# Kernel tuning notes

Measured on AMD Instinct MI355X. Metric: run time of the kernel, lower is better.

Reference implementation:

```python
import jax, jax.numpy as jnp
import numpy as np

VOCAB = 100000
EMB = 300      # embd_dim
S = 40         # sequence_length
B = 8192
C = 210        # out_channels
KH = 3         # kernel_height
DH = 35        # dense_hidden
NC = 35        # n_classes
KPOOL = S - KH + 1          # 38: MaxPool2d kernel height
NBLK = C // KPOOL           # 5: pool blocks over the channel dim (last 20 chans dropped)


def setup_inputs() -> dict:
    key = jax.random.key(0)
    ks = jax.random.split(key, 9)
    return {
        "x": jax.random.randint(ks[0], (B, S), 0, VOCAB, dtype=jnp.int64 if jax.config.jax_enable_x64 else jnp.int32),
        "pos_": jax.random.randint(ks[1], (B, 2), 0, S, dtype=jnp.int64 if jax.config.jax_enable_x64 else jnp.int32),
        "w2v": jax.random.normal(ks[2], (VOCAB, EMB), jnp.float32) * 0.1,
        "conv_w": jax.random.normal(ks[3], (KH, EMB, C), jnp.float32) * 0.02,   # WIO layout
        "conv_b": jax.random.normal(ks[4], (C,), jnp.float32) * 0.02,
        "dense_w": jax.random.normal(ks[5], (3 * S, DH), jnp.float32) * 0.05,
        "dense_b": jax.random.normal(ks[6], (DH,), jnp.float32) * 0.05,
        "out_w": jax.random.normal(ks[7], (DH, NC), jnp.float32) * 0.05,
        "out_b": jax.random.normal(ks[8], (NC,), jnp.float32) * 0.05,
    }


def reference(x, pos_, w2v, conv_w, conv_b, dense_w, dense_b, out_w, out_b):
    # Embedding lookup: [B, S, EMB]
    emb = w2v[x]
    # Conv2d(1, C, (KH, EMB), padding=(1, 0)) == 1D conv over seq with full-width kernel
    c = jax.lax.conv_general_dilated(
        emb, conv_w, window_strides=(1,), padding=[(1, 1)],
        dimension_numbers=("NWC", "WIO", "NWC"))  # [B, S, C]
    c = jax.nn.relu(c + conv_b)
    c = jnp.transpose(c, (0, 2, 1))  # [B, C, S], matches conv.squeeze(3)

    # ep1/ep2 normalization (faithful to the python loop)
    ep1 = jnp.minimum(pos_[:, 0], pos_[:, 1])
    ep2 = jnp.maximum(pos_[:, 0], pos_[:, 1])
    shift = (ep1 == 0).astype(ep1.dtype)
    ep1 = ep1 + shift
    ep2 = ep2 + shift

    pos = jnp.arange(S)
    m1 = (pos[None, :] < ep1[:, None]).astype(c.dtype)                                  # before e1
    m2 = ((pos[None, :] >= ep1[:, None]) & (pos[None, :] < ep2[:, None])).astype(c.dtype)  # between
    m3 = (pos[None, :] >= ep2[:, None]).astype(c.dtype)                                 # after e2

    def pool(m):
        # mask along seq, then MaxPool2d((38,1)) on a 3D tensor pools the CHANNEL dim
        y = c * m[:, None, :]                                  # [B, C, S]
        y = y[:, : NBLK * KPOOL, :].reshape(y.shape[0], NBLK, KPOOL, S)
        return y.max(axis=2)                                   # [B, NBLK, S]

    pooled = jnp.concatenate([pool(m1), pool(m2), pool(m3)], axis=2)  # [B, NBLK, 3S]
    pooled = pooled.reshape(-1, 3 * S)                                # [NBLK*B, 3S]
    h = pooled @ dense_w + dense_b
    return h @ out_w + out_b  # [NBLK*B, NC]
```

## Files before the change

kernel.cpp:

```cpp
#include <hip/hip_runtime.h>

typedef short bf16x8 __attribute__((ext_vector_type(8)));
typedef float f32x4 __attribute__((ext_vector_type(4)));
typedef unsigned short u16;
typedef u16 ushort8v __attribute__((ext_vector_type(8)));

#define VOCAB 100000
#define EMB 300
#define SEQ 40
#define BATCH 8192
#define COUT 210
#define NBLK 5
#define KPOOL 38
#define DH 35
#define NCLS 35
#define PCOL 320
#define KDIM 960
#define NUSE 192
#define BM 80
#define EROWS 84
#define NGR 120

__device__ __forceinline__ u16 f2bf(float f) {
  unsigned u = __float_as_uint(f);
  unsigned r = 0x7FFFu + ((u >> 16) & 1u);
  return (u16)((u + r) >> 16);
}

__device__ __forceinline__ void gload_lds16(void* lds, const void* g) {
  __builtin_amdgcn_global_load_lds(
      (const __attribute__((address_space(1))) void*)g,
      (__attribute__((address_space(3))) void*)lds, 16, 0, 0);
}

__global__ __launch_bounds__(256) void k_prepW(const float* __restrict__ w2v,
                                               u16* __restrict__ W) {
  int id = blockIdx.x * 256 + threadIdx.x;
  if (id >= (VOCAB + 1) * 40) return;
  int v = id / 40, e8 = id - v * 40;
  int e = e8 * 8;
  float vals[8] = {0.f, 0.f, 0.f, 0.f, 0.f, 0.f, 0.f, 0.f};
  if (v < VOCAB) {
    const float* src = w2v + (size_t)v * EMB + e;
    if (e <= 292) {
      float4 f0 = *(const float4*)src;
      float4 f1 = *(const float4*)(src + 4);
      vals[0] = f0.x; vals[1] = f0.y; vals[2] = f0.z; vals[3] = f0.w;
      vals[4] = f1.x; vals[5] = f1.y; vals[6] = f1.z; vals[7] = f1.w;
    } else if (e == 296) {
      float4 f0 = *(const float4*)src;
      vals[0] = f0.x; vals[1] = f0.y; vals[2] = f0.z; vals[3] = f0.w;
    }
  }
  ushort8v o;
#pragma unroll
  for (int j = 0; j < 8; ++j) o[j] = f2bf(vals[j]);
  *(ushort8v*)(W + (size_t)v * PCOL + e) = o;
}

__global__ __launch_bounds__(256) void k_prepB(const float* __restrict__ convw,
                                               u16* __restrict__ Btn) {
  int id = blockIdx.x * 256 + threadIdx.x;
  if (id >= NGR * NUSE) return;
  int gg = id / NUSE, col = id - gg * NUSE;
  ushort8v o;
#pragma unroll
  for (int j = 0; j < 8; ++j) {
    int k = gg * 8 + j;
    int kh = (k >= 640) ? 2 : (k >= 320 ? 1 : 0);
    int e = k - kh * PCOL;
    float v = (e < EMB) ? convw[(kh * EMB + e) * COUT + col] : 0.f;
    o[j] = f2bf(v);
  }
  *(ushort8v*)(Btn + (size_t)id * 8) = o;
}

__global__ __launch_bounds__(256) void k_conv_gemm(const u16* __restrict__ Wb,
                                                   const u16* __restrict__ Btn,
                                                   const int* __restrict__ x,
                                                   const float* __restrict__ convb,
                                                   float* __restrict__ maxc) {
  __shared__ __align__(16) char smem[40 * EROWS * 16];
  float* act = (float*)smem;

  const int tid = threadIdx.x;
  const int lane = tid & 63;
  const int wc = tid >> 6;
  const int l15 = lane & 15, l4 = lane >> 4;
  const int m0 = blockIdx.x * BM;
  const int b0 = blockIdx.x * 2;

#pragma unroll
  for (int ri = 0; ri < 13; ++ri) {
    const int c = ri * 256 + tid;
    const int g = c / 84;
    const int prow = c - g * 84;
    const int bb = (prow >= 42) ? 1 : 0;
    const int sp = prow - 42 * bb;
    const int tok = (sp == 0 || sp == 41) ? VOCAB : x[(b0 + bb) * SEQ + sp - 1];
    gload_lds16(smem + c * 16, Wb + (size_t)tok * PCOL + g * 8);
  }
  if (tid < 32) {
    const int c = 3328 + tid;
    const int g = c / 84;
    const int prow = c - g * 84;
    const int bb = (prow >= 42) ? 1 : 0;
    const int sp = prow - 42 * bb;
    const int tok = (sp == 0 || sp == 41) ? VOCAB : x[(b0 + bb) * SEQ + sp - 1];
    gload_lds16(smem + c * 16, Wb + (size_t)tok * PCOL + g * 8);
  }
  __syncthreads();

  const int rA0 = l15;
  const int rA1 = 16 + l15;
  const int rA2 = 32 + l15 + ((l15 >= 8) ? 2 : 0);
  const int rA3 = 50 + l15;
  const int rA4 = 66 + l15;

  const u16* pbB = Btn + (size_t)((l4 * NUSE) + wc * 48 + l15) * 8;

  f32x4 acc[5][3];
  const f32x4 zero = {0.f, 0.f, 0.f, 0.f};
#pragma unroll
  for (int i = 0; i < 5; ++i)
#pragma unroll
    for (int j = 0; j < 3; ++j) acc[i][j] = zero;

  bf16x8 bs[3][3];

#define LOADB(SI, T)                                                           \
  {                                                                            \
    const u16* p_ = pbB + (size_t)(T) * 6144;                                  \
    bs[SI][0] = *(const bf16x8*)(p_);                                          \
    bs[SI][1] = *(const bf16x8*)(p_ + 128);                                    \
    bs[SI][2] = *(const bf16x8*)(p_ + 256);                                    \
  }

  LOADB(0, 0)
  LOADB(1, 1)

#pragma unroll
  for (int kh = 0; kh < 3; ++kh) {
#pragma unroll
    for (int kq = 0; kq < 10; ++kq) {
      const int t = kh * 10 + kq;
      if (t + 2 < 30) LOADB((t + 2) % 3, t + 2)
      const char* kb = smem + ((kq * 4 + l4) * EROWS + kh) * 16;
      bf16x8 a0 = *(const bf16x8*)(kb + rA0 * 16);
      bf16x8 a1 = *(const bf16x8*)(kb + rA1 * 16);
      bf16x8 a2 = *(const bf16x8*)(kb + rA2 * 16);
      bf16x8 a3 = *(const bf16x8*)(kb + rA3 * 16);
      bf16x8 a4 = *(const bf16x8*)(kb + rA4 * 16);
      __builtin_amdgcn_s_setprio(1);
#pragma unroll
      for (int fn = 0; fn < 3; ++fn) {
        acc[0][fn] = __builtin_amdgcn_mfma_f32_16x16x32_bf16(a0, bs[t % 3][fn], acc[0][fn], 0, 0, 0);
        acc[1][fn] = __builtin_amdgcn_mfma_f32_16x16x32_bf16(a1, bs[t % 3][fn], acc[1][fn], 0, 0, 0);
        acc[2][fn] = __builtin_amdgcn_mfma_f32_16x16x32_bf16(a2, bs[t % 3][fn], acc[2][fn], 0, 0, 0);
        acc[3][fn] = __builtin_amdgcn_mfma_f32_16x16x32_bf16(a3, bs[t % 3][fn], acc[3][fn], 0, 0, 0);
        acc[4][fn] = __builtin_amdgcn_mfma_f32_16x16x32_bf16(a4, bs[t % 3][fn], acc[4][fn], 0, 0, 0);
      }
      __builtin_amdgcn_s_setprio(0);
    }
  }
#undef LOADB

  __syncthreads();

#pragma unroll
  for (int fm = 0; fm < 5; ++fm) {
#pragma unroll
    for (int fn = 0; fn < 3; ++fn) {
      const int col = wc * 48 + fn * 16 + l15;
      const float bias = convb[col];
#pragma unroll
      for (int rg = 0; rg < 4; ++rg) {
        const int rloc = l4 * 4 + rg;
        float vv = acc[fm][fn][rg] + bias;
        act[rloc * 194 + col] = fmaxf(vv, 0.f);
      }
    }
    __syncthreads();
    if (tid < 80) {
      const int rl = tid / 5, gq = tid - rl * 5;
      const float* ap = act + rl * 194 + gq * KPOOL;
      float mx = 0.f;
#pragma unroll
      for (int i = 0; i < KPOOL; ++i) mx = fmaxf(mx, ap[i]);
      const int mloc = fm * 16 + rl;
      const int bb = (mloc >= 40) ? 1 : 0;
      const int ss = mloc - 40 * bb;
      maxc[((b0 + bb) * NBLK + gq) * SEQ + ss] = mx;
    }
    __syncthreads();
  }
}

__global__ __launch_bounds__(256) void k_dense(const float* __restrict__ maxc,
                                               const int* __restrict__ pos,
                                               const float* __restrict__ dw,
                                               const float* __restrict__ db,
                                               const float* __restrict__ ow,
                                               const float* __restrict__ ob,
                                               float* __restrict__ out) {
  __shared__ float dwL[120 * 36];
  __shared__ float owL[35 * 36];
  __shared__ float hL[64 * 36];
  __shared__ float mxL[64 * 40];
  const int tid = threadIdx.x;
  const int r0 = blockIdx.x * 64;
  for (int i = tid; i < 120 * 35; i += 256) { int j = i / 35, d = i - j * 35; dwL[j * 36 + d] = dw[i]; }
  for (int i = tid; i < 35 * 35; i += 256)  { int j = i / 35, d = i - j * 35; owL[j * 36 + d] = ow[i]; }
  for (int i = tid; i < 64 * 40; i += 256)  mxL[i] = maxc[(size_t)r0 * 40 + i];
  __syncthreads();
  for (int t = tid; t < 64 * 35; t += 256) {
    const int row = t / 35, d = t - row * 35;
    const int rg = r0 + row;
    const int b = rg / NBLK;
    const int p0 = pos[b * 2], p1 = pos[b * 2 + 1];
    int e1 = min(p0, p1), e2 = max(p0, p1);
    if (e1 == 0) { e1 = 1; e2 += 1; }
    float a = db[d];
#pragma unroll
    for (int s = 0; s < SEQ; ++s) {
      const int k = (s >= e1) + (s >= e2);
      a += mxL[row * 40 + s] * dwL[(k * SEQ + s) * 36 + d];
    }
    hL[row * 36 + d] = a;
  }
  __syncthreads();
  for (int t = tid; t < 64 * 35; t += 256) {
    const int row = t / 35, c = t - row * 35;
    float a = ob[c];
#pragma unroll
    for (int d = 0; d < DH; ++d) a += hL[row * 36 + d] * owL[d * 36 + c];
    out[(size_t)(r0 + row) * NCLS + c] = a;
  }
}

extern "C" void kernel_launch(void* const* d_in, const int* in_sizes, int n_in,
                              void* d_out, int out_size, void* d_ws, size_t ws_size,
                              hipStream_t stream) {
  const int*   x     = (const int*)d_in[0];
  const int*   pos   = (const int*)d_in[1];
  const float* w2v   = (const float*)d_in[2];
  const float* convw = (const float*)d_in[3];
  const float* convb = (const float*)d_in[4];
  const float* dw    = (const float*)d_in[5];
  const float* db    = (const float*)d_in[6];
  const float* ow    = (const float*)d_in[7];
  const float* ob    = (const float*)d_in[8];
  float* out = (float*)d_out;

  char* ws = (char*)d_ws;
  u16* W    = (u16*)ws;
  u16* Btn  = (u16*)(ws + 64000640);
  float* maxc = (float*)(ws + 64000640 + 368640);

  k_prepW<<<15626, 256, 0, stream>>>(w2v, W);
  k_prepB<<<90, 256, 0, stream>>>(convw, Btn);
  k_conv_gemm<<<4096, 256, 0, stream>>>(W, Btn, x, convb, maxc);
  k_dense<<<640, 256, 0, stream>>>(maxc, pos, dw, db, ow, ob, out);
}
```

Baseline: 182.3 us.

## Retile conv GEMM to 128-row blocks with 32x32x16 MFMA and 8 waves

Restructures the conv GEMM kernel so each 512-thread block covers 128 output rows (spanning up to 5 batch items) instead of 80 rows. Each of the 8 waves now computes a 32x96 tile with 32x32x16 bf16 MFMAs, holding 3 accumulators instead of 15. A fragments are double-buffered from LDS and B fragments are prefetched from global memory two steps ahead. The aim is more reuse per A/B load and fewer, larger MFMA instructions. In exchange the LDS staging footprint roughly doubles (about 107 KB), which lowers the number of resident blocks, and the epilogue is serialized across the four row groups with extra barriers.

```diff
diff --git a/kernel.cpp b/kernel.cpp
--- a/kernel.cpp
+++ b/kernel.cpp
@@ -1,7 +1,7 @@
 #include <hip/hip_runtime.h>
 
 typedef short bf16x8 __attribute__((ext_vector_type(8)));
-typedef float f32x4 __attribute__((ext_vector_type(4)));
+typedef float f32x16 __attribute__((ext_vector_type(16)));
 typedef unsigned short u16;
 typedef u16 ushort8v __attribute__((ext_vector_type(8)));
 
@@ -15,10 +15,9 @@
 #define DH 35
 #define NCLS 35
 #define PCOL 320
-#define KDIM 960
 #define NUSE 192
-#define BM 80
-#define EROWS 84
+#define BM 128
+#define ER 168
 #define NGR 120
 
 __device__ __forceinline__ u16 f2bf(float f) {
@@ -75,122 +74,109 @@
   *(ushort8v*)(Btn + (size_t)id * 8) = o;
 }
 
-__global__ __launch_bounds__(256) void k_conv_gemm(const u16* __restrict__ Wb,
+__global__ __launch_bounds__(512) void k_conv_gemm(const u16* __restrict__ Wb,
                                                    const u16* __restrict__ Btn,
                                                    const int* __restrict__ x,
                                                    const float* __restrict__ convb,
                                                    float* __restrict__ maxc) {
-  __shared__ __align__(16) char smem[40 * EROWS * 16];
+  __shared__ __align__(16) char smem[40 * ER * 16];
   float* act = (float*)smem;
 
   const int tid = threadIdx.x;
   const int lane = tid & 63;
-  const int wc = tid >> 6;
-  const int l15 = lane & 15, l4 = lane >> 4;
+  const int w = tid >> 6;
+  const int wm = w >> 1, wn = w & 1;
+  const int l31 = lane & 31, h = lane >> 5;
   const int m0 = blockIdx.x * BM;
-  const int b0 = blockIdx.x * 2;
+  const int blo = m0 / SEQ;
 
 #pragma unroll
   for (int ri = 0; ri < 13; ++ri) {
-    const int c = ri * 256 + tid;
-    const int g = c / 84;
-    const int prow = c - g * 84;
-    const int bb = (prow >= 42) ? 1 : 0;
-    const int sp = prow - 42 * bb;
-    const int tok = (sp == 0 || sp == 41) ? VOCAB : x[(b0 + bb) * SEQ + sp - 1];
+    const int c = ri * 512 + tid;
+    const int g = c / ER, prow = c - g * ER;
+    const int bb = prow / 42, sp = prow - bb * 42;
+    const int tok = (sp == 0 || sp == 41) ? VOCAB : x[(blo + bb) * SEQ + sp - 1];
     gload_lds16(smem + c * 16, Wb + (size_t)tok * PCOL + g * 8);
   }
-  if (tid < 32) {
-    const int c = 3328 + tid;
-    const int g = c / 84;
-    const int prow = c - g * 84;
-    const int bb = (prow >= 42) ? 1 : 0;
-    const int sp = prow - 42 * bb;
-    const int tok = (sp == 0 || sp == 41) ? VOCAB : x[(b0 + bb) * SEQ + sp - 1];
+  if (tid < 64) {
+    const int c = 6656 + tid;
+    const int g = c / ER, prow = c - g * ER;
+    const int bb = prow / 42, sp = prow - bb * 42;
+    const int tok = (sp == 0 || sp == 41) ? VOCAB : x[(blo + bb) * SEQ + sp - 1];
     gload_lds16(smem + c * 16, Wb + (size_t)tok * PCOL + g * 8);
   }
-  __syncthreads();
-
-  const int rA0 = l15;
-  const int rA1 = 16 + l15;
-  const int rA2 = 32 + l15 + ((l15 >= 8) ? 2 : 0);
-  const int rA3 = 50 + l15;
-  const int rA4 = 66 + l15;
-
-  const u16* pbB = Btn + (size_t)((l4 * NUSE) + wc * 48 + l15) * 8;
-
-  f32x4 acc[5][3];
-  const f32x4 zero = {0.f, 0.f, 0.f, 0.f};
-#pragma unroll
-  for (int i = 0; i < 5; ++i)
-#pragma unroll
-    for (int j = 0; j < 3; ++j) acc[i][j] = zero;
-
-  bf16x8 bs[3][3];
+
+  int aBase;
+  {
+    const int m = m0 + wm * 32 + l31;
+    const int bA = m / SEQ, sA = m - bA * SEQ;
+    aBase = ((h * ER) + (bA - blo) * 42 + sA) * 16;
+  }
+  const int bElem = (h * NUSE + wn * 96 + l31) * 8;
+
+  f32x16 acc[3];
+  const f32x16 zero16 = {0.f,0.f,0.f,0.f,0.f,0.f,0.f,0.f,0.f,0.f,0.f,0.f,0.f,0.f,0.f,0.f};
+#pragma unroll
+  for (int j = 0; j < 3; ++j) acc[j] = zero16;
+
+  bf16x8 aR[2];
+  bf16x8 bS[3][3];
+
+#define LOADA(SLOT, T)                                                         \
+  aR[SLOT] = *(const bf16x8*)(smem + aBase + (((2 * (T)) % 40) * ER + (T) / 20) * 16);
 
 #define LOADB(SI, T)                                                           \
   {                                                                            \
-    const u16* p_ = pbB + (size_t)(T) * 6144;                                  \
-    bs[SI][0] = *(const bf16x8*)(p_);                                          \
-    bs[SI][1] = *(const bf16x8*)(p_ + 128);                                    \
-    bs[SI][2] = *(const bf16x8*)(p_ + 256);                                    \
+    const u16* p_ = Btn + (size_t)(T) * 3072 + bElem;                          \
+    bS[SI][0] = *(const bf16x8*)(p_);                                          \
+    bS[SI][1] = *(const bf16x8*)(p_ + 256);                                    \
+    bS[SI][2] = *(const bf16x8*)(p_ + 512);                                    \
   }
 
   LOADB(0, 0)
   LOADB(1, 1)
-
-#pragma unroll
-  for (int kh = 0; kh < 3; ++kh) {
-#pragma unroll
-    for (int kq = 0; kq < 10; ++kq) {
-      const int t = kh * 10 + kq;
-      if (t + 2 < 30) LOADB((t + 2) % 3, t + 2)
-      const char* kb = smem + ((kq * 4 + l4) * EROWS + kh) * 16;
-      bf16x8 a0 = *(const bf16x8*)(kb + rA0 * 16);
-      bf16x8 a1 = *(const bf16x8*)(kb + rA1 * 16);
-      bf16x8 a2 = *(const bf16x8*)(kb + rA2 * 16);
-      bf16x8 a3 = *(const bf16x8*)(kb + rA3 * 16);
-      bf16x8 a4 = *(const bf16x8*)(kb + rA4 * 16);
-      __builtin_amdgcn_s_setprio(1);
+  __syncthreads();
+  LOADA(0, 0)
+
+#pragma unroll
+  for (int t = 0; t < 60; ++t) {
+    if (t + 1 < 60) { LOADA((t + 1) & 1, t + 1) }
+    if (t + 2 < 60) { LOADB((t + 2) % 3, t + 2) }
+    __builtin_amdgcn_s_setprio(1);
+#pragma unroll
+    for (int fn = 0; fn < 3; ++fn)
+      acc[fn] = __builtin_amdgcn_mfma_f32_32x32x16_bf16(aR[t & 1], bS[t % 3][fn], acc[fn], 0, 0, 0);
+    __builtin_amdgcn_s_setprio(0);
+  }
+#undef LOADA
+#undef LOADB
+
+  __syncthreads();
+
+#pragma unroll
+  for (int ch = 0; ch < 4; ++ch) {
+    if (wm == ch) {
 #pragma unroll
       for (int fn = 0; fn < 3; ++fn) {
-        acc[0][fn] = __builtin_amdgcn_mfma_f32_16x16x32_bf16(a0, bs[t % 3][fn], acc[0][fn], 0, 0, 0);
-        acc[1][fn] = __builtin_amdgcn_mfma_f32_16x16x32_bf16(a1, bs[t % 3][fn], acc[1][fn], 0, 0, 0);
-        acc[2][fn] = __builtin_amdgcn_mfma_f32_16x16x32_bf16(a2, bs[t % 3][fn], acc[2][fn], 0, 0, 0);
-        acc[3][fn] = __builtin_amdgcn_mfma_f32_16x16x32_bf16(a3, bs[t % 3][fn], acc[3][fn], 0, 0, 0);
-        acc[4][fn] = __builtin_amdgcn_mfma_f32_16x16x32_bf16(a4, bs[t % 3][fn], acc[4][fn], 0, 0, 0);
+        const int col = wn * 96 + fn * 32 + l31;
+        const float bias = convb[col];
+#pragma unroll
+        for (int r = 0; r < 16; ++r) {
+          const int row = (r & 3) + 8 * (r >> 2) + 4 * h;
+          act[row * 194 + col] = fmaxf(acc[fn][r] + bias, 0.f);
+        }
       }
-      __builtin_amdgcn_s_setprio(0);
-    }
-  }
-#undef LOADB
-
-  __syncthreads();
-
-#pragma unroll
-  for (int fm = 0; fm < 5; ++fm) {
-#pragma unroll
-    for (int fn = 0; fn < 3; ++fn) {
-      const int col = wc * 48 + fn * 16 + l15;
-      const float bias = convb[col];
-#pragma unroll
-      for (int rg = 0; rg < 4; ++rg) {
-        const int rloc = l4 * 4 + rg;
-        float vv = acc[fm][fn][rg] + bias;
-        act[rloc * 194 + col] = fmaxf(vv, 0.f);
-      }
     }
     __syncthreads();
-    if (tid < 80) {
+    if (tid < 160) {
       const int rl = tid / 5, gq = tid - rl * 5;
       const float* ap = act + rl * 194 + gq * KPOOL;
       float mx = 0.f;
 #pragma unroll
       for (int i = 0; i < KPOOL; ++i) mx = fmaxf(mx, ap[i]);
-      const int mloc = fm * 16 + rl;
-      const int bb = (mloc >= 40) ? 1 : 0;
-      const int ss = mloc - 40 * bb;
-      maxc[((b0 + bb) * NBLK + gq) * SEQ + ss] = mx;
+      const int m = m0 + ch * 32 + rl;
+      const int bb = m / SEQ, ss = m - bb * SEQ;
+      maxc[(bb * NBLK + gq) * SEQ + ss] = mx;
     }
     __syncthreads();
   }
@@ -259,6 +245,6 @@
 
   k_prepW<<<15626, 256, 0, stream>>>(w2v, W);
   k_prepB<<<90, 256, 0, stream>>>(convw, Btn);
-  k_conv_gemm<<<4096, 256, 0, stream>>>(W, Btn, x, convb, maxc);
+  k_conv_gemm<<<2560, 512, 0, stream>>>(W, Btn, x, convb, maxc);
   k_dense<<<640, 256, 0, stream>>>(maxc, pos, dw, db, ow, ob, out);
 }
```

Result: slower. 272.2 us (+49.3%).
